# Kernel optimization log

Hardware: AMD Instinct MI355X
Metric: run time of the kernel (lower is better)

Reference implementation:

```python
import jax, jax.numpy as jnp
import numpy as np

K_NBR = 128        # PyG radius(max_num_neighbors=128)
NEG_FILL = -1e9    # mask value for max-aggregation over invalid neighbors


def fps(pos, m):
    # Farthest point sampling on pos [N,2] -> [m] int32 indices (start at 0).
    n = pos.shape[0]
    def step(carry, _):
        min_d2, last = carry
        d2 = jnp.sum((pos - pos[last]) ** 2, axis=-1)
        min_d2 = jnp.minimum(min_d2, d2)
        nxt = jnp.argmax(min_d2).astype(jnp.int32)
        return (min_d2, nxt), nxt
    init = (jnp.full((n,), 1e10, pos.dtype), jnp.int32(0))
    _, idxs = jax.lax.scan(step, init, None, length=m - 1)
    return jnp.concatenate([jnp.zeros((1,), jnp.int32), idxs])


def set_abstraction(x, pos, ratio, r, W, b):
    # x [B,N,C], pos [B,N,2]. FPS centers, radius neighbors (<=K), PointNetConv
    # message = Linear(cat[x_j, pos_j - pos_i]) (PyG MLP with one layer and
    # plain_last=True is a bare Linear), then max-aggregate per center.
    B, N, C = x.shape
    m = int(N * ratio)
    idx = jax.vmap(lambda p: fps(p, m))(pos)                         # [B,m]
    ctr = jnp.take_along_axis(pos, idx[..., None], axis=1)           # [B,m,2]
    d2 = jnp.sum((ctr[:, :, None, :] - pos[:, None, :, :]) ** 2, -1)  # [B,m,N]
    k = min(K_NBR, N)
    neg_d2, nbr = jax.lax.top_k(-d2, k)                              # [B,m,k]
    valid = (-neg_d2) <= r * r                                       # in-radius mask
    gather = jax.vmap(lambda a, i: a[i])                             # per-sample fancy index
    x_j = gather(x, nbr)                                             # [B,m,k,C]
    rel = gather(pos, nbr) - ctr[:, :, None, :]                      # [B,m,k,2]
    msg = jnp.concatenate([x_j, rel], axis=-1) @ W + b               # [B,m,k,F]
    msg = jnp.where(valid[..., None], msg, NEG_FILL)
    return jnp.max(msg, axis=2), ctr                                 # [B,m,F], [B,m,2]


def encoder(x, zones_ids, lf_W1, lf_b1, lf_W2, lf_b2, c1_W, c1_b, c2_W, c2_b, c3_W, c3_b):
    lf = jnp.tanh(jnp.tanh(x @ lf_W1 + lf_b1) @ lf_W2 + lf_b2)       # [B,N,64]
    h = jnp.concatenate([lf, zones_ids], axis=-1)                    # [B,N,65]
    h, pos = set_abstraction(h, x, 0.5, 0.5, c1_W, c1_b)             # [B,N/2,64]
    h, pos = set_abstraction(h, pos, 0.25, 1.0, c2_W, c2_b)          # [B,N/8,128]
    g = jnp.concatenate([h, pos], axis=-1) @ c3_W + c3_b             # [B,N/8,1024]
    gf = jnp.max(g, axis=1, keepdims=True)                           # global max pool -> [B,1,1024]
    return lf, gf


def setup_inputs():
    key = jax.random.key(0)
    ks = jax.random.split(key, 12)
    B, N = 4, 4096
    def lin(kw, kb, fi, fo):
        return (jax.random.normal(kw, (fi, fo), jnp.float32) / np.sqrt(fi),
                jax.random.normal(kb, (fo,), jnp.float32) * 0.01)
    x = jax.random.normal(ks[0], (B, N, 2), jnp.float32) * 4.0  # spread so ball(r) holds <128 pts
    zones_ids = jax.random.uniform(ks[1], (B, N, 1), jnp.float32)
    lf_W1, lf_b1 = lin(ks[2], ks[3], 2, 64)
    lf_W2, lf_b2 = lin(ks[4], ks[5], 64, 64)
    c1_W, c1_b = lin(ks[6], ks[7], 67, 64)
    c2_W, c2_b = lin(ks[8], ks[9], 66, 128)
    c3_W, c3_b = lin(ks[10], ks[11], 130, 1024)
    return {"x": x, "zones_ids": zones_ids, "lf_W1": lf_W1, "lf_b1": lf_b1,
            "lf_W2": lf_W2, "lf_b2": lf_b2, "c1_W": c1_W, "c1_b": c1_b,
            "c2_W": c2_W, "c2_b": c2_b, "c3_W": c3_W, "c3_b": c3_b}


def reference(x, zones_ids, lf_W1, lf_b1, lf_W2, lf_b2, c1_W, c1_b, c2_W, c2_b, c3_W, c3_b):
    return encoder(x, zones_ids, lf_W1, lf_b1, lf_W2, lf_b2,
                   c1_W, c1_b, c2_W, c2_b, c3_W, c3_b)
```

## Files before the change

kernel.cpp:

```cpp
#include <hip/hip_runtime.h>


constexpr int BB = 4;
constexpr int NN = 4096;
constexpr int M1 = 2048;
constexpr int M2 = 512;

typedef float v2f __attribute__((ext_vector_type(2)));

__device__ __forceinline__ float d2_exact(float dx, float dy) {
    return __fadd_rn(__fmul_rn(dx, dx), __fmul_rn(dy, dy));
}

template<int CTRL>
__device__ __forceinline__ unsigned dppz(unsigned v) {
    return (unsigned)__builtin_amdgcn_update_dpp(0, (int)v, CTRL, 0xF, 0xF, true);
}
template<int CTRL>
__device__ __forceinline__ float dppzf(float v) {
    return __uint_as_float(dppz<CTRL>(__float_as_uint(v)));
}
template<int CTRL>
__device__ __forceinline__ unsigned long long dpp64z(unsigned long long v) {
    unsigned lo = dppz<CTRL>((unsigned)v);
    unsigned hi = dppz<CTRL>((unsigned)(v >> 32));
    return ((unsigned long long)hi << 32) | (unsigned long long)lo;
}
template<int CTRL>
__device__ __forceinline__ void pairc(unsigned long long& t1, unsigned long long& t2) {
    unsigned long long o1 = dpp64z<CTRL>(t1);
    unsigned long long o2 = dpp64z<CTRL>(t2);
    bool g = o1 > t1;
    unsigned long long m1 = g ? o1 : t1;
    unsigned long long sm = g ? t1 : o1;
    unsigned long long cn = g ? o2 : t2;
    t2 = cn > sm ? cn : sm;
    t1 = m1;
}
__device__ __forceinline__ unsigned long long readlane64(unsigned long long v, int l) {
    unsigned lo = (unsigned)__builtin_amdgcn_readlane((int)(unsigned)v, l);
    unsigned hi = (unsigned)__builtin_amdgcn_readlane((int)(unsigned)(v >> 32), l);
    return ((unsigned long long)hi << 32) | (unsigned long long)lo;
}
__device__ __forceinline__ float wave_fmax_nn(float v) {
    v = fmaxf(v, dppzf<0x111>(v)); v = fmaxf(v, dppzf<0x112>(v));
    v = fmaxf(v, dppzf<0x114>(v)); v = fmaxf(v, dppzf<0x118>(v));
    v = fmaxf(v, dppzf<0x142>(v)); v = fmaxf(v, dppzf<0x143>(v));
    return v;
}
__device__ __forceinline__ unsigned wave_umax_z(unsigned v) {
    unsigned o;
    o = dppz<0x111>(v); v = o > v ? o : v;
    o = dppz<0x112>(v); v = o > v ? o : v;
    o = dppz<0x114>(v); v = o > v ? o : v;
    o = dppz<0x118>(v); v = o > v ? o : v;
    o = dppz<0x142>(v); v = o > v ? o : v;
    o = dppz<0x143>(v); v = o > v ? o : v;
    return v;
}

__global__ __launch_bounds__(256) void k_lf_y1(
    const float2* __restrict__ x, const float* __restrict__ zones,
    const float* __restrict__ W1, const float* __restrict__ b1,
    const float* __restrict__ W2, const float* __restrict__ b2,
    const float* __restrict__ c1W, const float* __restrict__ c1b,
    float* __restrict__ out_lf, float* __restrict__ y1)
{
    __shared__ float sh[4][64];
    __shared__ float sl[4][64];
    int tid = threadIdx.x;
    int p = tid >> 6, f = tid & 63;
    size_t pt = (size_t)blockIdx.x * 4 + p;
    float2 xv = x[pt];
    float hid = tanhf(xv.x * W1[f] + xv.y * W1[64 + f] + b1[f]);
    sh[p][f] = hid;
    __syncthreads();
    float acc = b2[f];
#pragma unroll
    for (int c = 0; c < 64; ++c) acc += sh[p][c] * W2[c * 64 + f];
    float lf = tanhf(acc);
    sl[p][f] = lf;
    out_lf[pt * 64 + f] = lf;
    __syncthreads();
    float acc2 = c1b[f] + zones[pt] * c1W[64 * 64 + f]
               + xv.x * c1W[65 * 64 + f] + xv.y * c1W[66 * 64 + f];
#pragma unroll
    for (int c = 0; c < 64; ++c) acc2 += sl[p][c] * c1W[c * 64 + f];
    y1[pt * 64 + f] = acc2;
}

template<int M, int PPT>
__device__ __forceinline__ void fps_core(
    const float2* __restrict__ src, const float2* __restrict__ PTSl,
    float2* __restrict__ centl, unsigned long long (&slk)[2][8],
    int tid, int lane, int wv)
{
#pragma clang fp contract(off)
    constexpr int PP2 = PPT / 2;
    v2f px2[PP2], py2[PP2], md2[PP2];
#pragma unroll
    for (int k = 0; k < PP2; ++k) {
        float2 a = src[tid + (2 * k) * 256];
        float2 b = src[tid + (2 * k + 1) * 256];
        px2[k] = (v2f){a.x, b.x};
        py2[k] = (v2f){a.y, b.y};
        md2[k] = (v2f){1e10f, 1e10f};
    }
    float2 c0 = src[0];
    if (tid == 0) centl[0] = c0;

    float c1x = c0.x, c1y = c0.y, c2x = 0.0f, c2y = 0.0f;
    bool two = false;
    int it = 1;
    unsigned rc = 0;
    while (it < M) {
        int par = (int)(rc & 1u); ++rc;
        v2f vcx = (v2f){c1x, c1x}, vcy = (v2f){c1y, c1y};
#pragma unroll
        for (int k = 0; k < PP2; ++k) {
            v2f dx = px2[k] - vcx, dy = py2[k] - vcy;
            v2f d2 = (dx * dx) + (dy * dy);
            md2[k] = __builtin_elementwise_min(md2[k], d2);
        }
        if (two) {
            v2f wcx = (v2f){c2x, c2x}, wcy = (v2f){c2y, c2y};
#pragma unroll
            for (int k = 0; k < PP2; ++k) {
                v2f dx = px2[k] - wcx, dy = py2[k] - wcy;
                v2f d2 = (dx * dx) + (dy * dy);
                md2[k] = __builtin_elementwise_min(md2[k], d2);
            }
        }
        unsigned long long t1 = 0ull, t2 = 0ull;
#pragma unroll
        for (int s = 0; s < PPT; ++s) {
            float mq = (s & 1) ? md2[s >> 1].y : md2[s >> 1].x;
            unsigned long long key =
                ((unsigned long long)__float_as_uint(mq) << 32)
                | (unsigned long long)(0xFFFFFFFFu - (unsigned)(tid + s * 256));
            bool g = key > t1;
            unsigned long long ns = g ? t1 : (key > t2 ? key : t2);
            t1 = g ? key : t1;
            t2 = ns;
        }
        pairc<0x111>(t1, t2); pairc<0x112>(t1, t2); pairc<0x114>(t1, t2);
        pairc<0x118>(t1, t2); pairc<0x142>(t1, t2); pairc<0x143>(t1, t2);
        if (lane == 63) { slk[par][2 * wv] = t1; slk[par][2 * wv + 1] = t2; }
        __syncthreads();
        unsigned long long a1 = slk[par][2 * (lane & 3)];
        unsigned long long a2 = slk[par][2 * (lane & 3) + 1];
        if (lane >= 4) { a1 = 0ull; a2 = 0ull; }
        pairc<0x111>(a1, a2); pairc<0x112>(a1, a2);
        unsigned long long w1 = readlane64(a1, 3);
        unsigned long long r1 = readlane64(a2, 3);
        int jw = (int)(0xFFFFFFFFu - (unsigned)w1);
        int jr = (int)(0xFFFFFFFFu - (unsigned)r1);
        float mdr = __uint_as_float((unsigned)(r1 >> 32));
        float2 wpt = PTSl[jw];
        float2 rpt = PTSl[jr];
        float ddx = rpt.x - wpt.x, ddy = rpt.y - wpt.y;
        float dd = (ddx * ddx) + (ddy * ddy);
        bool dbl = (it + 1 < M) && (dd >= mdr);
        if (tid == 0) { centl[it] = wpt; if (dbl) centl[it + 1] = rpt; }
        c1x = wpt.x; c1y = wpt.y; c2x = rpt.x; c2y = rpt.y;
        two = dbl;
        it += dbl ? 2 : 1;
    }
}

template<int M, int PPT>
__device__ __forceinline__ void fps_core_sw(
    const float2* __restrict__ src, float2* __restrict__ centl, int lane)
{
#pragma clang fp contract(off)
    constexpr int PP2 = PPT / 2;
    v2f px2[PP2], py2[PP2], md2[PP2];
#pragma unroll
    for (int k = 0; k < PP2; ++k) {
        float2 a = src[lane + (2 * k) * 64];
        float2 b = src[lane + (2 * k + 1) * 64];
        px2[k] = (v2f){a.x, b.x};
        py2[k] = (v2f){a.y, b.y};
        md2[k] = (v2f){1e10f, 1e10f};
    }
    float2 c0 = src[0];
    float cx = c0.x, cy = c0.y;
    if (lane == 0) centl[0] = c0;

    for (int it = 1; it < M; ++it) {
        v2f vcx = (v2f){cx, cx}, vcy = (v2f){cy, cy};
        v2f mx = (v2f){0.0f, 0.0f};
#pragma unroll
        for (int k = 0; k < PP2; ++k) {
            v2f dx = px2[k] - vcx, dy = py2[k] - vcy;
            v2f d2 = (dx * dx) + (dy * dy);
            md2[k] = __builtin_elementwise_min(md2[k], d2);
            mx = __builtin_elementwise_max(mx, md2[k]);
        }
        float bm = fmaxf(mx.x, mx.y);
        float bmv = __uint_as_float((unsigned)__builtin_amdgcn_readlane(
            (int)__float_as_uint(wave_fmax_nn(bm)), 63));
        unsigned lk = 0u;
#pragma unroll
        for (int s = 0; s < PPT; ++s) {
            float mq = (s & 1) ? md2[s >> 1].y : md2[s >> 1].x;
            unsigned cand = 0xFFFFFFFFu - (unsigned)(lane + s * 64);
            lk = (mq == bmv && cand > lk) ? cand : lk;
        }
        unsigned wlo = (unsigned)__builtin_amdgcn_readlane((int)wave_umax_z(lk), 63);
        int j = (int)(0xFFFFFFFFu - wlo);
        float2 c = src[j];
        cx = c.x; cy = c.y;
        if (lane == 0) centl[it] = c;
    }
}

__global__ __launch_bounds__(256, 1) void k_fps_fused(
    const float2* __restrict__ pos, float* __restrict__ p1out,
    float* __restrict__ p2out)
{
    __shared__ float2 PTS[NN];
    __shared__ float2 cent1[M1];
    __shared__ float2 cent2[M2];
    __shared__ unsigned long long slk[2][8];
    int tid = threadIdx.x, lane = tid & 63, wv = tid >> 6;
    const float2* p = pos + (size_t)blockIdx.x * NN;

    for (int i = tid; i < NN; i += 256) PTS[i] = p[i];
    __syncthreads();

    fps_core<M1, NN / 256>(p, PTS, cent1, slk, tid, lane, wv);
    __syncthreads();
    float2* o1 = (float2*)(p1out + (size_t)blockIdx.x * M1 * 2);
    for (int i = tid; i < M1; i += 256) o1[i] = cent1[i];

    if (wv == 0)
        fps_core_sw<M2, M1 / 64>(cent1, cent2, lane);
    __syncthreads();
    float2* o2 = (float2*)(p2out + (size_t)blockIdx.x * M2 * 2);
    for (int i = tid; i < M2; i += 256) o2[i] = cent2[i];
}

__global__ __launch_bounds__(256) void k_sa(
    const float2* __restrict__ candpos, const float* __restrict__ y,
    const float* __restrict__ ctr, const float* __restrict__ W,
    int NP, int F, int relrow, float r2, float* __restrict__ hout)
{
    __shared__ int cnt;
    __shared__ int list[4096];
    int tid = threadIdx.x;
    int b = blockIdx.y;
    size_t crow = (size_t)b * gridDim.x + blockIdx.x;
    if (tid == 0) cnt = 0;
    __syncthreads();
    float cx = ctr[crow * 2], cy = ctr[crow * 2 + 1];
    const float2* cp = candpos + (size_t)b * NP;
    for (int j = tid; j < NP; j += 256) {
        float2 pj = cp[j];
        float d2 = d2_exact(pj.x - cx, pj.y - cy);
        if (d2 <= r2) { int t = atomicAdd(&cnt, 1); list[t] = j; }
    }
    __syncthreads();
    int n = cnt;
    for (int f = tid; f < F; f += 256) {
        float m = -3.0e38f;
        for (int t = 0; t < n; ++t)
            m = fmaxf(m, y[((size_t)b * NP + list[t]) * F + f]);
        float ct = cx * W[(size_t)relrow * F + f] + cy * W[(size_t)(relrow + 1) * F + f];
        hout[crow * F + f] = m - ct;
    }
}

__global__ __launch_bounds__(128) void k_y2(
    const float* __restrict__ h1, const float* __restrict__ p1,
    const float* __restrict__ W, const float* __restrict__ bb,
    float* __restrict__ y2)
{
    __shared__ float sh[64];
    size_t row = blockIdx.x;
    int f = threadIdx.x;
    if (f < 64) sh[f] = h1[row * 64 + f];
    __syncthreads();
    float acc = bb[f] + p1[row * 2] * W[64 * 128 + f]
              + p1[row * 2 + 1] * W[65 * 128 + f];
#pragma unroll
    for (int c = 0; c < 64; ++c) acc += sh[c] * W[c * 128 + f];
    y2[row * 128 + f] = acc;
}

__global__ __launch_bounds__(256) void k_g(
    const float* __restrict__ h2, const float* __restrict__ p2,
    const float* __restrict__ W3, const float* __restrict__ b3,
    float* __restrict__ part)
{
    int f = blockIdx.x * 256 + threadIdx.x;
    int b = blockIdx.z;
    int i0 = blockIdx.y * 8;
    float acc[8];
    float bbv = b3[f];
#pragma unroll
    for (int ii = 0; ii < 8; ++ii) acc[ii] = bbv;
    const float* hrow = h2 + ((size_t)b * M2 + i0) * 128;
    for (int c = 0; c < 128; ++c) {
        float w = W3[(size_t)c * 1024 + f];
#pragma unroll
        for (int ii = 0; ii < 8; ++ii) acc[ii] += hrow[ii * 128 + c] * w;
    }
    float wx = W3[(size_t)128 * 1024 + f];
    float wy = W3[(size_t)129 * 1024 + f];
    const float* prow = p2 + ((size_t)b * M2 + i0) * 2;
    float m = -3.0e38f;
#pragma unroll
    for (int ii = 0; ii < 8; ++ii) {
        float g = acc[ii] + prow[ii * 2] * wx + prow[ii * 2 + 1] * wy;
        m = fmaxf(m, g);
    }
    part[((size_t)b * 64 + blockIdx.y) * 1024 + f] = m;
}

__global__ __launch_bounds__(256) void k_gmax(const float* __restrict__ part,
                                              float* __restrict__ outg)
{
    int f = blockIdx.x * 256 + threadIdx.x;
    int b = f >> 10, fl = f & 1023;
    float m = -3.0e38f;
#pragma unroll 8
    for (int ig = 0; ig < 64; ++ig)
        m = fmaxf(m, part[((size_t)b * 64 + ig) * 1024 + fl]);
    outg[f] = m;
}

extern "C" void kernel_launch(void* const* d_in, const int* in_sizes, int n_in,
                              void* d_out, int out_size, void* d_ws, size_t ws_size,
                              hipStream_t stream)
{
    const float* x    = (const float*)d_in[0];
    const float* zon  = (const float*)d_in[1];
    const float* lfW1 = (const float*)d_in[2];
    const float* lfb1 = (const float*)d_in[3];
    const float* lfW2 = (const float*)d_in[4];
    const float* lfb2 = (const float*)d_in[5];
    const float* c1W  = (const float*)d_in[6];
    const float* c1b  = (const float*)d_in[7];
    const float* c2W  = (const float*)d_in[8];
    const float* c2b  = (const float*)d_in[9];
    const float* c3W  = (const float*)d_in[10];
    const float* c3b  = (const float*)d_in[11];
    float* out = (float*)d_out;

    char* w = (char*)d_ws;
    float* big = (float*)w;                    w += (size_t)BB * NN * 64 * 4;
    float* p1  = (float*)w;                    w += (size_t)BB * M1 * 2 * 4;
    float* h1  = (float*)w;                    w += (size_t)BB * M1 * 64 * 4;
    float* p2  = (float*)w;                    w += (size_t)BB * M2 * 2 * 4;
    float* h2  = (float*)w;                    w += (size_t)BB * M2 * 128 * 4;
    float* y1 = big, * y2 = big, * part = big;

    k_lf_y1<<<BB * NN / 4, 256, 0, stream>>>((const float2*)x, zon, lfW1, lfb1,
                                             lfW2, lfb2, c1W, c1b, out, y1);
    k_fps_fused<<<BB, 256, 0, stream>>>((const float2*)x, p1, p2);
    k_sa<<<dim3(M1, BB), 256, 0, stream>>>((const float2*)x, y1, p1, c1W,
                                           NN, 64, 65, 0.25f, h1);
    k_y2<<<BB * M1, 128, 0, stream>>>(h1, p1, c2W, c2b, y2);
    k_sa<<<dim3(M2, BB), 256, 0, stream>>>((const float2*)p1, y2, p2, c2W,
                                           M1, 128, 64, 1.0f, h2);
    k_g<<<dim3(4, 64, BB), 256, 0, stream>>>(h2, p2, c3W, c3b, part);
    k_gmax<<<16, 256, 0, stream>>>(part, out + (size_t)BB * NN * 64);
}
```

Before: 1.707 ms.

## Speculatively pick two FPS centers per iteration using top-2 wave reduction

The single-wave FPS loop now tracks the top-2 (distance, index) keys per lane and merges them with a DPP pairwise reduction. After each round it checks whether the runner-up would still be the farthest point once the winner is applied (its distance to the winner is at least its current min distance). If so, it emits both centers in one iteration and applies both distance updates in the next pass. This cuts the number of serial reduction rounds, at the cost of a heavier 64-bit top-2 reduction and an extra update pass when doubling occurs.

Result: no change. 1.734 ms (+1.6%).

```diff
diff --git a/kernel.cpp b/kernel.cpp
--- a/kernel.cpp
+++ b/kernel.cpp
@@ -15,10 +15,6 @@
 template<int CTRL>
 __device__ __forceinline__ unsigned dppz(unsigned v) {
     return (unsigned)__builtin_amdgcn_update_dpp(0, (int)v, CTRL, 0xF, 0xF, true);
-}
-template<int CTRL>
-__device__ __forceinline__ float dppzf(float v) {
-    return __uint_as_float(dppz<CTRL>(__float_as_uint(v)));
 }
 template<int CTRL>
 __device__ __forceinline__ unsigned long long dpp64z(unsigned long long v) {
@@ -41,22 +37,6 @@
     unsigned lo = (unsigned)__builtin_amdgcn_readlane((int)(unsigned)v, l);
     unsigned hi = (unsigned)__builtin_amdgcn_readlane((int)(unsigned)(v >> 32), l);
     return ((unsigned long long)hi << 32) | (unsigned long long)lo;
-}
-__device__ __forceinline__ float wave_fmax_nn(float v) {
-    v = fmaxf(v, dppzf<0x111>(v)); v = fmaxf(v, dppzf<0x112>(v));
-    v = fmaxf(v, dppzf<0x114>(v)); v = fmaxf(v, dppzf<0x118>(v));
-    v = fmaxf(v, dppzf<0x142>(v)); v = fmaxf(v, dppzf<0x143>(v));
-    return v;
-}
-__device__ __forceinline__ unsigned wave_umax_z(unsigned v) {
-    unsigned o;
-    o = dppz<0x111>(v); v = o > v ? o : v;
-    o = dppz<0x112>(v); v = o > v ? o : v;
-    o = dppz<0x114>(v); v = o > v ? o : v;
-    o = dppz<0x118>(v); v = o > v ? o : v;
-    o = dppz<0x142>(v); v = o > v ? o : v;
-    o = dppz<0x143>(v); v = o > v ? o : v;
-    return v;
 }
 
 __global__ __launch_bounds__(256) void k_lf_y1(
@@ -184,34 +164,56 @@
         md2[k] = (v2f){1e10f, 1e10f};
     }
     float2 c0 = src[0];
-    float cx = c0.x, cy = c0.y;
     if (lane == 0) centl[0] = c0;
 
-    for (int it = 1; it < M; ++it) {
-        v2f vcx = (v2f){cx, cx}, vcy = (v2f){cy, cy};
-        v2f mx = (v2f){0.0f, 0.0f};
+    float c1x = c0.x, c1y = c0.y, c2x = 0.0f, c2y = 0.0f;
+    bool two = false;
+    int it = 1;
+    while (it < M) {
+        v2f vcx = (v2f){c1x, c1x}, vcy = (v2f){c1y, c1y};
 #pragma unroll
         for (int k = 0; k < PP2; ++k) {
             v2f dx = px2[k] - vcx, dy = py2[k] - vcy;
             v2f d2 = (dx * dx) + (dy * dy);
             md2[k] = __builtin_elementwise_min(md2[k], d2);
-            mx = __builtin_elementwise_max(mx, md2[k]);
-        }
-        float bm = fmaxf(mx.x, mx.y);
-        float bmv = __uint_as_float((unsigned)__builtin_amdgcn_readlane(
-            (int)__float_as_uint(wave_fmax_nn(bm)), 63));
-        unsigned lk = 0u;
+        }
+        if (two) {
+            v2f wcx = (v2f){c2x, c2x}, wcy = (v2f){c2y, c2y};
+#pragma unroll
+            for (int k = 0; k < PP2; ++k) {
+                v2f dx = px2[k] - wcx, dy = py2[k] - wcy;
+                v2f d2 = (dx * dx) + (dy * dy);
+                md2[k] = __builtin_elementwise_min(md2[k], d2);
+            }
+        }
+        unsigned long long t1 = 0ull, t2 = 0ull;
 #pragma unroll
         for (int s = 0; s < PPT; ++s) {
             float mq = (s & 1) ? md2[s >> 1].y : md2[s >> 1].x;
-            unsigned cand = 0xFFFFFFFFu - (unsigned)(lane + s * 64);
-            lk = (mq == bmv && cand > lk) ? cand : lk;
-        }
-        unsigned wlo = (unsigned)__builtin_amdgcn_readlane((int)wave_umax_z(lk), 63);
-        int j = (int)(0xFFFFFFFFu - wlo);
-        float2 c = src[j];
-        cx = c.x; cy = c.y;
-        if (lane == 0) centl[it] = c;
+            unsigned long long key =
+                ((unsigned long long)__float_as_uint(mq) << 32)
+                | (unsigned long long)(0xFFFFFFFFu - (unsigned)(lane + s * 64));
+            bool g = key > t1;
+            unsigned long long ns = g ? t1 : (key > t2 ? key : t2);
+            t1 = g ? key : t1;
+            t2 = ns;
+        }
+        pairc<0x111>(t1, t2); pairc<0x112>(t1, t2); pairc<0x114>(t1, t2);
+        pairc<0x118>(t1, t2); pairc<0x142>(t1, t2); pairc<0x143>(t1, t2);
+        unsigned long long w1 = readlane64(t1, 63);
+        unsigned long long r1 = readlane64(t2, 63);
+        int jw = (int)(0xFFFFFFFFu - (unsigned)w1);
+        int jr = (int)(0xFFFFFFFFu - (unsigned)r1);
+        float mdr = __uint_as_float((unsigned)(r1 >> 32));
+        float2 wpt = src[jw];
+        float2 rpt = src[jr];
+        float ddx = rpt.x - wpt.x, ddy = rpt.y - wpt.y;
+        float dd = (ddx * ddx) + (ddy * ddy);
+        bool dbl = (it + 1 < M) && (dd >= mdr);
+        if (lane == 0) { centl[it] = wpt; if (dbl) centl[it + 1] = rpt; }
+        c1x = wpt.x; c1y = wpt.y; c2x = rpt.x; c2y = rpt.y;
+        two = dbl;
+        it += dbl ? 2 : 1;
     }
 }
 
```
